# Performance work log

Measured on AMD Instinct MI355X. Metric: run time of the kernel, lower is better.

Reference implementation:

```python
import jax, jax.numpy as jnp
import numpy as np
import math

N = 100000
D = 128       # input_dim
DK = 32       # d_k
H = 4         # heads
DV = D // H   # d_v = 32
DFF = 512     # 4 * input_dim
EPS = 1e-5


def layer_norm(x, g, b):
    mu = jnp.mean(x, axis=-1, keepdims=True)
    var = jnp.var(x, axis=-1, keepdims=True)
    return (x - mu) * jax.lax.rsqrt(var + EPS) * g + b


def setup_inputs() -> dict:
    key = jax.random.key(0)
    ks = jax.random.split(key, 10)
    x = jax.random.normal(ks[0], (N, D), dtype=jnp.float32)
    neighbor_index = jax.random.randint(ks[1], (N, 4), 0, N)
    # xavier-ish scaled params
    w_q = jax.random.normal(ks[2], (H, D, DK), dtype=jnp.float32) * math.sqrt(2.0 / (D + DK))
    w_k = jax.random.normal(ks[3], (H, 5, D, DK), dtype=jnp.float32) * math.sqrt(2.0 / (D + DK))
    w_v = jax.random.normal(ks[4], (H, 5, D, DV), dtype=jnp.float32) * math.sqrt(2.0 / (D + DV))
    W1 = jax.random.normal(ks[5], (D, DFF), dtype=jnp.float32) * math.sqrt(1.0 / D)
    b1 = jnp.zeros((DFF,), dtype=jnp.float32)
    W2 = jax.random.normal(ks[6], (DFF, D), dtype=jnp.float32) * math.sqrt(1.0 / DFF)
    b2 = jnp.zeros((D,), dtype=jnp.float32)
    g1 = jnp.ones((D,), dtype=jnp.float32)
    beta1 = jnp.zeros((D,), dtype=jnp.float32)
    g2 = jnp.ones((D,), dtype=jnp.float32)
    beta2 = jnp.zeros((D,), dtype=jnp.float32)
    return {"x": x, "neighbor_index": neighbor_index, "w_q": w_q, "w_k": w_k,
            "w_v": w_v, "W1": W1, "b1": b1, "W2": W2, "b2": b2,
            "g1": g1, "beta1": beta1, "g2": g2, "beta2": beta2}


def attention(x, neighbor_index, w_q, w_k, w_v):
    # gather the 4 typed neighbors and prepend the self node -> (N, 5, D)
    x_nb = jnp.concatenate([x[:, None, :], x[neighbor_index]], axis=1)
    Q = jnp.einsum('nd,hdk->hnk', x, w_q)                 # (H, N, DK)
    K = jnp.einsum('nrd,hrdk->hnrk', x_nb, w_k)           # (H, N, 5, DK)
    V = jnp.einsum('nrd,hrdv->hnrv', x_nb, w_v)           # (H, N, 5, DV)
    A = jnp.einsum('hnk,hnrk->hnr', Q, K) / math.sqrt(DK)
    # NOTE: original torch code applies softmax over dim=1 (the node axis),
    # reproduced faithfully here.
    A = jax.nn.softmax(A, axis=1)
    Z = jnp.einsum('hnr,hnrv->hnv', A, V)                 # (H, N, DV)
    return jnp.transpose(Z, (1, 0, 2)).reshape(x.shape[0], -1)  # (N, H*DV)


def reference(x, neighbor_index, w_q, w_k, w_v, W1, b1, W2, b2, g1, beta1, g2, beta2):
    attn = attention(x, neighbor_index, w_q, w_k, w_v)
    h = layer_norm(x + attn, g1, beta1)
    ffn = jax.nn.relu(h @ W1 + b1) @ W2 + b2
    return layer_norm(h + ffn, g2, beta2)
```

## Files before the change

### kernel.cpp

```cpp
#include <hip/hip_runtime.h>
#include <hip/hip_bf16.h>

typedef unsigned short u16;
typedef __attribute__((ext_vector_type(8))) short short8;
typedef __attribute__((ext_vector_type(4))) float f32x4;
typedef __attribute__((ext_vector_type(4))) float float4v;
typedef __attribute__((ext_vector_type(4))) unsigned short us4;

#define NN       100000
#define OFF_WK   16384
#define OFF_WV   98304
#define OFF_W1   180224
#define OFF_W2   245760
#define PACK_ELEMS 311296

#define WS_LWS   0u
#define WS_PM    8000000u
#define WS_PS    8000640u
#define WS_MHR   8001280u
#define WS_ISHR  8001408u
#define WS_PK    8001536u
#define WS_XB    8624128u
#define WS_SV    34224128u

static __device__ __forceinline__ float b2f(u16 u){
  unsigned int i = ((unsigned int)u) << 16;
  float f; __builtin_memcpy(&f, &i, 4); return f;
}
static __device__ __forceinline__ u16 f2b(float f){
  unsigned int i; __builtin_memcpy(&i, &f, 4);
  i += 0x7FFFu + ((i >> 16) & 1u);
  return (u16)(i >> 16);
}
static __device__ __forceinline__ f32x4 mfma16(short8 a, short8 b, f32x4 c){
  return __builtin_amdgcn_mfma_f32_16x16x32_bf16(a, b, c, 0, 0, 0);
}
static __device__ __forceinline__ bool detect32(const void* g1){
  return ((const u16*)g1)[0] == 0;
}
static __device__ __forceinline__ float ldf(const void* p, size_t i, bool is32){
  return is32 ? ((const float*)p)[i] : b2f(((const u16*)p)[i]);
}

__global__ __launch_bounds__(256) void k_convert_x(
    const void* __restrict__ x, const void* __restrict__ g1, u16* __restrict__ xb)
{
  const bool is32 = detect32(g1);
  size_t i = (size_t)blockIdx.x * 256 + threadIdx.x;
  us4 o;
  if (is32){
    float4v v = ((const float4v*)x)[i];
    o.x = f2b(v.x); o.y = f2b(v.y); o.z = f2b(v.z); o.w = f2b(v.w);
  } else {
    o = ((const us4*)x)[i];
  }
  ((us4*)xb)[i] = o;
}

__global__ __launch_bounds__(256) void k_convert_small(
    const void* b1, const void* b2, const void* g1, const void* be1,
    const void* g2, const void* be2, u16* __restrict__ sv)
{
  const bool is32 = detect32(g1);
  for (int i = threadIdx.x; i < 1152; i += 256){
    const void* src; int off;
    if      (i < 512) { src = b1;  off = i; }
    else if (i < 640) { src = b2;  off = i - 512; }
    else if (i < 768) { src = g1;  off = i - 640; }
    else if (i < 896) { src = be1; off = i - 768; }
    else if (i < 1024){ src = g2;  off = i - 896; }
    else              { src = be2; off = i - 1024; }
    sv[i] = f2b(ldf(src, off, is32));
  }
}

__global__ __launch_bounds__(256) void k_pack(
    const void* __restrict__ wq, const void* __restrict__ wk,
    const void* __restrict__ wv, const void* __restrict__ W1,
    const void* __restrict__ W2, const void* __restrict__ g1,
    u16* __restrict__ pk)
{
  const bool is32 = detect32(g1);
  int p = blockIdx.x * 256 + threadIdx.x;
  if (p >= PACK_ELEMS) return;
  float v;
  if (p < OFF_WK){
    int q = p;
    int j = q & 7, lane = (q >> 3) & 63, tk = q >> 9;
    int kb = tk & 3, t = tk >> 2;
    int kd = kb*32 + (lane>>4)*8 + j, nc = t*16 + (lane & 15);
    v = ldf(wq, (size_t)(nc>>5)*4096 + kd*32 + (nc & 31), is32);
  } else if (p < OFF_WV){
    int q = p - OFF_WK; int r = q >> 14; q &= 16383;
    int j = q & 7, lane = (q >> 3) & 63, tk = q >> 9;
    int kb = tk & 3, t = tk >> 2;
    int kd = kb*32 + (lane>>4)*8 + j, nc = t*16 + (lane & 15);
    v = ldf(wk, (size_t)((nc>>5)*5 + r)*4096 + kd*32 + (nc & 31), is32);
  } else if (p < OFF_W1){
    int q = p - OFF_WV; int r = q >> 14; q &= 16383;
    int j = q & 7, lane = (q >> 3) & 63, tk = q >> 9;
    int kb = tk & 3, t = tk >> 2;
    int kd = kb*32 + (lane>>4)*8 + j, nc = t*16 + (lane & 15);
    v = ldf(wv, (size_t)((nc>>5)*5 + r)*4096 + kd*32 + (nc & 31), is32);
  } else if (p < OFF_W2){
    int q = p - OFF_W1;
    int j = q & 7, lane = (q >> 3) & 63, tk = q >> 9;
    int kb = tk & 3, t = tk >> 2;
    int kd = kb*32 + (lane>>4)*8 + j, nc = t*16 + (lane & 15);
    v = ldf(W1, (size_t)kd*512 + nc, is32);
  } else {
    int q = p - OFF_W2;
    int j = q & 7, lane = (q >> 3) & 63, tk = q >> 9;
    int c = tk >> 5, t = (tk >> 2) & 7, kb2 = tk & 3;
    int kd = (c*4+kb2)*32 + (lane>>4)*8 + j, nc = t*16 + (lane & 15);
    v = ldf(W2, (size_t)kd*128 + nc, is32);
  }
  pk[p] = f2b(v);
}

__global__ __launch_bounds__(256) void k_qk(
    const u16* __restrict__ x, const int* __restrict__ nbr,
    const u16* __restrict__ pw, float* __restrict__ lws)
{
  __shared__ __align__(16) u16 sbuf[16384];
  const int tid = threadIdx.x, lane = tid & 63, wv = tid >> 6;
  const int m = lane & 15, quad = lane >> 4;
  const int n0 = blockIdx.x * 64 + wv * 16;
  const bool act = (n0 < NN);

  for (int s = tid; s < 2048; s += 256)
    ((short8*)sbuf)[s] = ((const short8*)pw)[s];
  __syncthreads();

  short8 a_self[4];
  f32x4 q[8];
  #pragma unroll
  for (int t = 0; t < 8; t++) q[t] = (f32x4){0.f,0.f,0.f,0.f};
  if (act){
    const short8* xp = (const short8*)(x + (size_t)(n0 + m) * 128);
    #pragma unroll
    for (int kb = 0; kb < 4; kb++) a_self[kb] = xp[kb*4 + quad];
    #pragma unroll
    for (int t = 0; t < 8; t++)
      #pragma unroll
      for (int kb = 0; kb < 4; kb++)
        q[t] = mfma16(a_self[kb], ((const short8*)sbuf)[(t*4+kb)*64 + lane], q[t]);
  }

  for (int r = 0; r < 5; r++){
    __syncthreads();
    for (int s = tid; s < 2048; s += 256)
      ((short8*)sbuf)[s] = ((const short8*)(pw + OFF_WK + (size_t)r*16384))[s];
    __syncthreads();
    if (act){
      short8 a[4];
      if (r == 0){
        #pragma unroll
        for (int kb = 0; kb < 4; kb++) a[kb] = a_self[kb];
      } else {
        int node = nbr[(size_t)(n0 + m)*4 + (r-1)];
        const short8* xp = (const short8*)(x + (size_t)node * 128);
        #pragma unroll
        for (int kb = 0; kb < 4; kb++) a[kb] = xp[kb*4 + quad];
      }
      #pragma unroll
      for (int h = 0; h < 4; h++){
        f32x4 k0 = {0.f,0.f,0.f,0.f}, k1 = {0.f,0.f,0.f,0.f};
        #pragma unroll
        for (int kb = 0; kb < 4; kb++){
          k0 = mfma16(a[kb], ((const short8*)sbuf)[((2*h  )*4+kb)*64 + lane], k0);
          k1 = mfma16(a[kb], ((const short8*)sbuf)[((2*h+1)*4+kb)*64 + lane], k1);
        }
        float p[4];
        #pragma unroll
        for (int i = 0; i < 4; i++) p[i] = q[2*h][i]*k0[i] + q[2*h+1][i]*k1[i];
        #pragma unroll
        for (int mask = 1; mask < 16; mask <<= 1){
          #pragma unroll
          for (int i = 0; i < 4; i++) p[i] += __shfl_xor(p[i], mask, 16);
        }
        if (m == 0){
          #pragma unroll
          for (int i = 0; i < 4; i++)
            lws[(size_t)(h*5+r)*NN + n0 + quad*4 + i] = p[i] * 0.17677669529663687f;
        }
      }
    }
  }
}

__global__ __launch_bounds__(256) void k_red_part(
    const float* __restrict__ lws, float* __restrict__ pm, float* __restrict__ ps)
{
  const int hr = blockIdx.x >> 3, pb = blockIdx.x & 7;
  const int start = pb * 12500, end = start + 12500;
  const float* v = lws + (size_t)hr * NN;
  __shared__ float red[256];
  float mx = -1e30f;
  for (int i = start + threadIdx.x; i < end; i += 256) mx = fmaxf(mx, v[i]);
  red[threadIdx.x] = mx; __syncthreads();
  for (int s = 128; s > 0; s >>= 1){
    if ((int)threadIdx.x < s) red[threadIdx.x] = fmaxf(red[threadIdx.x], red[threadIdx.x+s]);
    __syncthreads();
  }
  mx = red[0]; __syncthreads();
  float sm = 0.f;
  for (int i = start + threadIdx.x; i < end; i += 256) sm += __expf(v[i] - mx);
  red[threadIdx.x] = sm; __syncthreads();
  for (int s = 128; s > 0; s >>= 1){
    if ((int)threadIdx.x < s) red[threadIdx.x] += red[threadIdx.x+s];
    __syncthreads();
  }
  if (threadIdx.x == 0){ pm[blockIdx.x] = mx; ps[blockIdx.x] = red[0]; }
}

__global__ __launch_bounds__(64) void k_red_fin(
    const float* __restrict__ pm, const float* __restrict__ ps,
    float* __restrict__ mhr, float* __restrict__ ishr)
{
  int t = threadIdx.x;
  if (t < 20){
    float M = -1e30f;
    for (int b = 0; b < 8; b++) M = fmaxf(M, pm[t*8+b]);
    float S = 0.f;
    for (int b = 0; b < 8; b++) S += ps[t*8+b] * __expf(pm[t*8+b] - M);
    mhr[t] = M; ishr[t] = 1.0f / S;
  }
}

__global__ __launch_bounds__(256, 2) void k_attn_ffn(
    const u16* __restrict__ x, const void* __restrict__ xraw,
    const int* __restrict__ nbr,
    const u16* __restrict__ pw, const float* __restrict__ lws,
    const float* __restrict__ mhr, const float* __restrict__ ishr,
    const u16* __restrict__ sv, const void* __restrict__ g1raw,
    float* __restrict__ out)
{
  __shared__ __align__(16) u16 sbuf[16384];
  __shared__ __align__(16) u16 hgbuf[16384];
  __shared__ float attw[2560];
  const int tid = threadIdx.x, lane = tid & 63, wv = tid >> 6;
  const int m = lane & 15, quad = lane >> 4;
  const int nblk = blockIdx.x * 128;
  const int n0 = nblk + wv * 32;
  const bool act0 = (n0 < NN), act1 = (n0 + 16 < NN);
  const bool is32 = detect32(g1raw);
  const u16* b1s = sv;
  const u16* b2s = sv + 512;
  const u16* g1s = sv + 640;
  const u16* be1s = sv + 768;
  const u16* g2s = sv + 896;
  const u16* be2s = sv + 1024;

  for (int idx = tid; idx < 2560; idx += 256){
    int tile = idx / 320, rem = idx - tile*320;
    int r = rem >> 6, h = (rem >> 4) & 3, mm = rem & 15, hr = h*5 + r;
    int node = nblk + tile*16 + mm;
    attw[idx] = (node < NN)
        ? __expf(lws[(size_t)hr*NN + node] - mhr[hr]) * ishr[hr] : 0.f;
  }

  f32x4 zacc[2][8];
  #pragma unroll
  for (int tl = 0; tl < 2; tl++)
    #pragma unroll
    for (int t = 0; t < 8; t++) zacc[tl][t] = (f32x4){0.f,0.f,0.f,0.f};

  for (int r = 0; r < 5; r++){
    __syncthreads();
    for (int s = tid; s < 2048; s += 256)
      ((short8*)sbuf)[s] = ((const short8*)(pw + OFF_WV + (size_t)r*16384))[s];
    __syncthreads();

    short8 a2[2][4];
    #pragma unroll
    for (int tl = 0; tl < 2; tl++){
      bool act = tl ? act1 : act0;
      if (!act) continue;
      int rowb = n0 + tl*16;
      if (r == 0){
        const short8* xp = (const short8*)(x + (size_t)(rowb + m) * 128);
        #pragma unroll
        for (int kb = 0; kb < 4; kb++) a2[tl][kb] = xp[kb*4 + quad];
      } else {
        int node = nbr[(size_t)(rowb + m)*4 + (r-1)];
        const short8* xp = (const short8*)(x + (size_t)node * 128);
        #pragma unroll
        for (int kb = 0; kb < 4; kb++) a2[tl][kb] = xp[kb*4 + quad];
      }
    }
    #pragma unroll
    for (int t = 0; t < 8; t++){
      short8 bfr[4];
      #pragma unroll
      for (int kb = 0; kb < 4; kb++)
        bfr[kb] = ((const short8*)sbuf)[(t*4+kb)*64 + lane];
      int h = t >> 1;
      #pragma unroll
      for (int tl = 0; tl < 2; tl++){
        bool act = tl ? act1 : act0;
        if (!act) continue;
        f32x4 v = {0.f,0.f,0.f,0.f};
        #pragma unroll
        for (int kb = 0; kb < 4; kb++) v = mfma16(a2[tl][kb], bfr[kb], v);
        const float* aw = attw + (wv*2+tl)*320 + (r*4+h)*16;
        #pragma unroll
        for (int i = 0; i < 4; i++) zacc[tl][t][i] += aw[quad*4+i] * v[i];
      }
    }
  }
  __syncthreads();

  unsigned int hDp[2][8][2];
  #pragma unroll
  for (int tl = 0; tl < 2; tl++){
    bool act = tl ? act1 : act0;
    if (!act) continue;
    int rowb = n0 + tl*16;
    #pragma unroll
    for (int t = 0; t < 8; t++)
      #pragma unroll
      for (int i = 0; i < 4; i++)
        zacc[tl][t][i] += ldf(xraw, (size_t)(rowb + quad*4 + i)*128 + t*16 + m, is32);
    float s1[4] = {0,0,0,0}, s2[4] = {0,0,0,0};
    #pragma unroll
    for (int t = 0; t < 8; t++)
      #pragma unroll
      for (int i = 0; i < 4; i++){ float y = zacc[tl][t][i]; s1[i] += y; s2[i] += y*y; }
    #pragma unroll
    for (int mask = 1; mask < 16; mask <<= 1){
      #pragma unroll
      for (int i = 0; i < 4; i++){
        s1[i] += __shfl_xor(s1[i], mask, 16);
        s2[i] += __shfl_xor(s2[i], mask, 16);
      }
    }
    float mu[4], rs[4];
    #pragma unroll
    for (int i = 0; i < 4; i++){
      mu[i] = s1[i] * (1.f/128.f);
      float var = s2[i] * (1.f/128.f) - mu[i]*mu[i];
      rs[i] = rsqrtf(var + 1e-5f);
    }
    #pragma unroll
    for (int t = 0; t < 8; t++){
      float gg = b2f(g1s[t*16+m]), bb = b2f(be1s[t*16+m]);
      u16 hv[4];
      #pragma unroll
      for (int i = 0; i < 4; i++){
        hv[i] = f2b((zacc[tl][t][i]-mu[i])*rs[i]*gg + bb);
        hgbuf[(size_t)(wv*32 + tl*16 + quad*4 + i)*128 + t*16 + m] = hv[i];
      }
      hDp[tl][t][0] = (unsigned int)hv[0] | ((unsigned int)hv[1] << 16);
      hDp[tl][t][1] = (unsigned int)hv[2] | ((unsigned int)hv[3] << 16);
    }
  }
  __syncthreads();

  short8 ah[2][4];
  #pragma unroll
  for (int tl = 0; tl < 2; tl++){
    bool act = tl ? act1 : act0;
    if (!act) continue;
    #pragma unroll
    for (int kb = 0; kb < 4; kb++)
      ah[tl][kb] = ((const short8*)hgbuf)[(wv*32 + tl*16 + m)*16 + kb*4 + quad];
  }

  f32x4 f2acc[2][8];
  #pragma unroll
  for (int tl = 0; tl < 2; tl++)
    #pragma unroll
    for (int t = 0; t < 8; t++) f2acc[tl][t] = (f32x4){0.f,0.f,0.f,0.f};

  for (int c = 0; c < 4; c++){
    __syncthreads();
    for (int s = tid; s < 2048; s += 256)
      ((short8*)sbuf)[s] = ((const short8*)(pw + OFF_W1 + (size_t)c*16384))[s];
    __syncthreads();
    #pragma unroll
    for (int t2 = 0; t2 < 8; t2++){
      short8 bfr[4];
      #pragma unroll
      for (int kb = 0; kb < 4; kb++)
        bfr[kb] = ((const short8*)sbuf)[(t2*4+kb)*64 + lane];
      float b1c = b2f(b1s[(c*8+t2)*16 + m]);
      #pragma unroll
      for (int tl = 0; tl < 2; tl++){
        bool act = tl ? act1 : act0;
        if (!act) continue;
        f32x4 g = {0.f,0.f,0.f,0.f};
        #pragma unroll
        for (int kb = 0; kb < 4; kb++) g = mfma16(ah[tl][kb], bfr[kb], g);
        #pragma unroll
        for (int i = 0; i < 4; i++)
          hgbuf[(size_t)(wv*32 + tl*16 + quad*4 + i)*128 + t2*16 + m]
              = f2b(fmaxf(g[i] + b1c, 0.f));
      }
    }
    __syncthreads();
    for (int s = tid; s < 2048; s += 256)
      ((short8*)sbuf)[s] = ((const short8*)(pw + OFF_W2 + (size_t)c*16384))[s];
    short8 ag[2][4];
    #pragma unroll
    for (int tl = 0; tl < 2; tl++){
      bool act = tl ? act1 : act0;
      if (!act) continue;
      #pragma unroll
      for (int kb2 = 0; kb2 < 4; kb2++)
        ag[tl][kb2] = ((const short8*)hgbuf)[(wv*32 + tl*16 + m)*16 + kb2*4 + quad];
    }
    __syncthreads();
    #pragma unroll
    for (int t = 0; t < 8; t++){
      short8 bfr[4];
      #pragma unroll
      for (int kb2 = 0; kb2 < 4; kb2++)
        bfr[kb2] = ((const short8*)sbuf)[(t*4+kb2)*64 + lane];
      #pragma unroll
      for (int tl = 0; tl < 2; tl++){
        bool act = tl ? act1 : act0;
        if (!act) continue;
        #pragma unroll
        for (int kb2 = 0; kb2 < 4; kb2++)
          f2acc[tl][t] = mfma16(ag[tl][kb2], bfr[kb2], f2acc[tl][t]);
      }
    }
  }

  #pragma unroll
  for (int tl = 0; tl < 2; tl++){
    bool act = tl ? act1 : act0;
    if (!act) continue;
    int rowb = n0 + tl*16;
    #pragma unroll
    for (int t = 0; t < 8; t++){
      float b2c = b2f(b2s[t*16 + m]);
      f2acc[tl][t][0] += b2f((u16)(hDp[tl][t][0] & 0xffff)) + b2c;
      f2acc[tl][t][1] += b2f((u16)(hDp[tl][t][0] >> 16))    + b2c;
      f2acc[tl][t][2] += b2f((u16)(hDp[tl][t][1] & 0xffff)) + b2c;
      f2acc[tl][t][3] += b2f((u16)(hDp[tl][t][1] >> 16))    + b2c;
    }
    float s1[4] = {0,0,0,0}, s2[4] = {0,0,0,0};
    #pragma unroll
    for (int t = 0; t < 8; t++)
      #pragma unroll
      for (int i = 0; i < 4; i++){ float y = f2acc[tl][t][i]; s1[i] += y; s2[i] += y*y; }
    #pragma unroll
    for (int mask = 1; mask < 16; mask <<= 1){
      #pragma unroll
      for (int i = 0; i < 4; i++){
        s1[i] += __shfl_xor(s1[i], mask, 16);
        s2[i] += __shfl_xor(s2[i], mask, 16);
      }
    }
    float mu2[4], rs2[4];
    #pragma unroll
    for (int i = 0; i < 4; i++){
      mu2[i] = s1[i] * (1.f/128.f);
      float var = s2[i] * (1.f/128.f) - mu2[i]*mu2[i];
      rs2[i] = rsqrtf(var + 1e-5f);
    }
    #pragma unroll
    for (int t = 0; t < 8; t++){
      float gg = b2f(g2s[t*16+m]), bb = b2f(be2s[t*16+m]);
      #pragma unroll
      for (int i = 0; i < 4; i++)
        out[(size_t)(rowb + quad*4 + i)*128 + t*16 + m] =
            (f2acc[tl][t][i]-mu2[i])*rs2[i]*gg + bb;
    }
  }
}

extern "C" void kernel_launch(void* const* d_in, const int* in_sizes, int n_in,
                              void* d_out, int out_size, void* d_ws, size_t ws_size,
                              hipStream_t stream)
{
  const void* x   = d_in[0];
  const int*  nbr = (const int*)d_in[1];
  const void* wq  = d_in[2];
  const void* wk  = d_in[3];
  const void* wv  = d_in[4];
  const void* W1  = d_in[5];
  const void* b1  = d_in[6];
  const void* W2  = d_in[7];
  const void* b2  = d_in[8];
  const void* g1  = d_in[9];
  const void* be1 = d_in[10];
  const void* g2  = d_in[11];
  const void* be2 = d_in[12];
  float* out = (float*)d_out;

  char* ws = (char*)d_ws;
  float* lws  = (float*)(ws + WS_LWS);
  float* pm   = (float*)(ws + WS_PM);
  float* ps   = (float*)(ws + WS_PS);
  float* mhr  = (float*)(ws + WS_MHR);
  float* ishr = (float*)(ws + WS_ISHR);
  u16*   pk   = (u16*)  (ws + WS_PK);
  u16*   xb   = (u16*)  (ws + WS_XB);
  u16*   sv   = (u16*)  (ws + WS_SV);

  k_convert_x<<<dim3(12500), dim3(256), 0, stream>>>(x, g1, xb);
  k_convert_small<<<dim3(1), dim3(256), 0, stream>>>(b1, b2, g1, be1, g2, be2, sv);
  k_pack<<<dim3((PACK_ELEMS+255)/256), dim3(256), 0, stream>>>(wq, wk, wv, W1, W2, g1, pk);
  k_qk<<<dim3((NN+63)/64), dim3(256), 0, stream>>>(xb, nbr, pk, lws);
  k_red_part<<<dim3(160), dim3(256), 0, stream>>>(lws, pm, ps);
  k_red_fin<<<dim3(1), dim3(64), 0, stream>>>(pm, ps, mhr, ishr);
  k_attn_ffn<<<dim3((NN+127)/128), dim3(256), 0, stream>>>(xb, x, nbr, pk, lws, mhr, ishr,
                                                           sv, g1, out);
}
```

Measured before the change: 314.0 us.

## Fuse FFN chunks through per-wave LDS slices and double rows per wave in QK

The QK kernel now processes 32 rows per wave (two 16-row tiles), so each weight fragment read from shared memory is reused across both tiles, and the grid is halved. The attention+FFN kernel drops its large shared hidden buffer and instead streams W1/W2 fragments interleaved per 32-column slice. Each wave writes its ReLU output into a small padded private LDS slice and immediately feeds it to the W2 MFMAs. The weight packing is reordered to match. This cuts shared memory per block to allow three blocks per CU and removes block-wide syncs around the hidden buffer, at the cost of more weight reload rounds and higher register pressure under the tighter launch bounds.

```diff
diff --git a/kernel.cpp b/kernel.cpp
--- a/kernel.cpp
+++ b/kernel.cpp
@@ -6,12 +6,12 @@
 typedef __attribute__((ext_vector_type(4))) float f32x4;
 typedef __attribute__((ext_vector_type(4))) float float4v;
 typedef __attribute__((ext_vector_type(4))) unsigned short us4;
+typedef __attribute__((ext_vector_type(2))) unsigned int uint2v;
 
 #define NN       100000
 #define OFF_WK   16384
 #define OFF_WV   98304
 #define OFF_W1   180224
-#define OFF_W2   245760
 #define PACK_ELEMS 311296
 
 #define WS_LWS   0u
@@ -23,6 +23,9 @@
 #define WS_XB    8624128u
 #define WS_SV    34224128u
 
+#define PWS_PITCH 36
+#define PWS_SLICE 1280
+
 static __device__ __forceinline__ float b2f(u16 u){
   unsigned int i = ((unsigned int)u) << 16;
   float f; __builtin_memcpy(&f, &i, 4); return f;
@@ -40,6 +43,14 @@
 }
 static __device__ __forceinline__ float ldf(const void* p, size_t i, bool is32){
   return is32 ? ((const float*)p)[i] : b2f(((const u16*)p)[i]);
+}
+static __device__ __forceinline__ short8 lds_afrag(const u16* p){
+  uint2v a = *(const uint2v*)p;
+  uint2v b = *(const uint2v*)(p + 4);
+  short8 r;
+  unsigned int* rp = (unsigned int*)&r;
+  rp[0] = a.x; rp[1] = a.y; rp[2] = b.x; rp[3] = b.y;
+  return r;
 }
 
 __global__ __launch_bounds__(256) void k_convert_x(
@@ -102,49 +113,67 @@
     int kb = tk & 3, t = tk >> 2;
     int kd = kb*32 + (lane>>4)*8 + j, nc = t*16 + (lane & 15);
     v = ldf(wv, (size_t)((nc>>5)*5 + r)*4096 + kd*32 + (nc & 31), is32);
-  } else if (p < OFF_W2){
+  } else {
     int q = p - OFF_W1;
-    int j = q & 7, lane = (q >> 3) & 63, tk = q >> 9;
-    int kb = tk & 3, t = tk >> 2;
-    int kd = kb*32 + (lane>>4)*8 + j, nc = t*16 + (lane & 15);
-    v = ldf(W1, (size_t)kd*512 + nc, is32);
-  } else {
-    int q = p - OFF_W2;
-    int j = q & 7, lane = (q >> 3) & 63, tk = q >> 9;
-    int c = tk >> 5, t = (tk >> 2) & 7, kb2 = tk & 3;
-    int kd = (c*4+kb2)*32 + (lane>>4)*8 + j, nc = t*16 + (lane & 15);
-    v = ldf(W2, (size_t)kd*128 + nc, is32);
+    int j = q & 7, lane = (q >> 3) & 63, rest = q >> 9;
+    int pairIdx = rest >> 4, sub = rest & 15;
+    int c = pairIdx >> 2, kb2 = pairIdx & 3;
+    int half = lane >> 4, mc = lane & 15;
+    if (sub < 8){
+      int u = sub >> 2, kb = sub & 3;
+      int kd = kb*32 + half*8 + j;
+      int nc = c*128 + (kb2*2+u)*16 + mc;
+      v = ldf(W1, (size_t)kd*512 + nc, is32);
+    } else {
+      int t = sub - 8;
+      int kd = (c*4+kb2)*32 + half*8 + j;
+      int nc = t*16 + mc;
+      v = ldf(W2, (size_t)kd*128 + nc, is32);
+    }
   }
   pk[p] = f2b(v);
 }
 
-__global__ __launch_bounds__(256) void k_qk(
+__global__ __launch_bounds__(256, 3) void k_qk(
     const u16* __restrict__ x, const int* __restrict__ nbr,
     const u16* __restrict__ pw, float* __restrict__ lws)
 {
   __shared__ __align__(16) u16 sbuf[16384];
   const int tid = threadIdx.x, lane = tid & 63, wv = tid >> 6;
   const int m = lane & 15, quad = lane >> 4;
-  const int n0 = blockIdx.x * 64 + wv * 16;
-  const bool act = (n0 < NN);
-
+  const int n0 = blockIdx.x * 128 + wv * 32;
+  const bool act0 = (n0 < NN), act1 = (n0 + 16 < NN);
+
+  const short8* sb8 = (const short8*)sbuf;
   for (int s = tid; s < 2048; s += 256)
     ((short8*)sbuf)[s] = ((const short8*)pw)[s];
   __syncthreads();
 
-  short8 a_self[4];
-  f32x4 q[8];
-  #pragma unroll
-  for (int t = 0; t < 8; t++) q[t] = (f32x4){0.f,0.f,0.f,0.f};
-  if (act){
-    const short8* xp = (const short8*)(x + (size_t)(n0 + m) * 128);
-    #pragma unroll
-    for (int kb = 0; kb < 4; kb++) a_self[kb] = xp[kb*4 + quad];
-    #pragma unroll
-    for (int t = 0; t < 8; t++)
-      #pragma unroll
-      for (int kb = 0; kb < 4; kb++)
-        q[t] = mfma16(a_self[kb], ((const short8*)sbuf)[(t*4+kb)*64 + lane], q[t]);
+  short8 a[2][4];
+  f32x4 q[2][8];
+  #pragma unroll
+  for (int tl = 0; tl < 2; tl++)
+    #pragma unroll
+    for (int t = 0; t < 8; t++) q[tl][t] = (f32x4){0.f,0.f,0.f,0.f};
+
+  #pragma unroll
+  for (int tl = 0; tl < 2; tl++){
+    if (!(tl ? act1 : act0)) continue;
+    const short8* xp = (const short8*)(x + (size_t)(n0 + tl*16 + m) * 128);
+    #pragma unroll
+    for (int kb = 0; kb < 4; kb++) a[tl][kb] = xp[kb*4 + quad];
+  }
+  #pragma unroll
+  for (int t = 0; t < 8; t++){
+    short8 bfr[4];
+    #pragma unroll
+    for (int kb = 0; kb < 4; kb++) bfr[kb] = sb8[(t*4+kb)*64 + lane];
+    #pragma unroll
+    for (int tl = 0; tl < 2; tl++){
+      if (!(tl ? act1 : act0)) continue;
+      #pragma unroll
+      for (int kb = 0; kb < 4; kb++) q[tl][t] = mfma16(a[tl][kb], bfr[kb], q[tl][t]);
+    }
   }
 
   for (int r = 0; r < 5; r++){
@@ -152,28 +181,36 @@
     for (int s = tid; s < 2048; s += 256)
       ((short8*)sbuf)[s] = ((const short8*)(pw + OFF_WK + (size_t)r*16384))[s];
     __syncthreads();
-    if (act){
-      short8 a[4];
-      if (r == 0){
-        #pragma unroll
-        for (int kb = 0; kb < 4; kb++) a[kb] = a_self[kb];
-      } else {
-        int node = nbr[(size_t)(n0 + m)*4 + (r-1)];
+    if (r > 0){
+      #pragma unroll
+      for (int tl = 0; tl < 2; tl++){
+        if (!(tl ? act1 : act0)) continue;
+        int node = nbr[(size_t)(n0 + tl*16 + m)*4 + (r-1)];
         const short8* xp = (const short8*)(x + (size_t)node * 128);
         #pragma unroll
-        for (int kb = 0; kb < 4; kb++) a[kb] = xp[kb*4 + quad];
-      }
-      #pragma unroll
-      for (int h = 0; h < 4; h++){
+        for (int kb = 0; kb < 4; kb++) a[tl][kb] = xp[kb*4 + quad];
+      }
+    }
+    #pragma unroll
+    for (int h = 0; h < 4; h++){
+      short8 b0[4], b1f[4];
+      #pragma unroll
+      for (int kb = 0; kb < 4; kb++){
+        b0[kb]  = sb8[((2*h  )*4+kb)*64 + lane];
+        b1f[kb] = sb8[((2*h+1)*4+kb)*64 + lane];
+      }
+      #pragma unroll
+      for (int tl = 0; tl < 2; tl++){
+        if (!(tl ? act1 : act0)) continue;
         f32x4 k0 = {0.f,0.f,0.f,0.f}, k1 = {0.f,0.f,0.f,0.f};
         #pragma unroll
         for (int kb = 0; kb < 4; kb++){
-          k0 = mfma16(a[kb], ((const short8*)sbuf)[((2*h  )*4+kb)*64 + lane], k0);
-          k1 = mfma16(a[kb], ((const short8*)sbuf)[((2*h+1)*4+kb)*64 + lane], k1);
+          k0 = mfma16(a[tl][kb], b0[kb],  k0);
+          k1 = mfma16(a[tl][kb], b1f[kb], k1);
         }
         float p[4];
         #pragma unroll
-        for (int i = 0; i < 4; i++) p[i] = q[2*h][i]*k0[i] + q[2*h+1][i]*k1[i];
+        for (int i = 0; i < 4; i++) p[i] = q[tl][2*h][i]*k0[i] + q[tl][2*h+1][i]*k1[i];
         #pragma unroll
         for (int mask = 1; mask < 16; mask <<= 1){
           #pragma unroll
@@ -182,7 +219,8 @@
         if (m == 0){
           #pragma unroll
           for (int i = 0; i < 4; i++)
-            lws[(size_t)(h*5+r)*NN + n0 + quad*4 + i] = p[i] * 0.17677669529663687f;
+            lws[(size_t)(h*5+r)*NN + n0 + tl*16 + quad*4 + i]
+                = p[i] * 0.17677669529663687f;
         }
       }
     }
@@ -228,7 +266,7 @@
   }
 }
 
-__global__ __launch_bounds__(256, 2) void k_attn_ffn(
+__global__ __launch_bounds__(256, 3) void k_attn_ffn(
     const u16* __restrict__ x, const void* __restrict__ xraw,
     const int* __restrict__ nbr,
     const u16* __restrict__ pw, const float* __restrict__ lws,
@@ -237,12 +275,10 @@
     float* __restrict__ out)
 {
   __shared__ __align__(16) u16 sbuf[16384];
-  __shared__ __align__(16) u16 hgbuf[16384];
-  __shared__ float attw[2560];
+  __shared__ __align__(16) u16 upool[5120];
   const int tid = threadIdx.x, lane = tid & 63, wv = tid >> 6;
   const int m = lane & 15, quad = lane >> 4;
-  const int nblk = blockIdx.x * 128;
-  const int n0 = nblk + wv * 32;
+  const int n0 = blockIdx.x * 128 + wv * 32;
   const bool act0 = (n0 < NN), act1 = (n0 + 16 < NN);
   const bool is32 = detect32(g1raw);
   const u16* b1s = sv;
@@ -251,12 +287,15 @@
   const u16* be1s = sv + 768;
   const u16* g2s = sv + 896;
   const u16* be2s = sv + 1024;
-
-  for (int idx = tid; idx < 2560; idx += 256){
-    int tile = idx / 320, rem = idx - tile*320;
+  const short8* sb8 = (const short8*)sbuf;
+  float* attw_w = ((float*)upool) + wv * 640;
+  u16*   pws_w  = upool + wv * PWS_SLICE;
+
+  for (int j = lane; j < 640; j += 64){
+    int tl = j / 320, rem = j - tl*320;
     int r = rem >> 6, h = (rem >> 4) & 3, mm = rem & 15, hr = h*5 + r;
-    int node = nblk + tile*16 + mm;
-    attw[idx] = (node < NN)
+    int node = n0 + tl*16 + mm;
+    attw_w[j] = (node < NN)
         ? __expf(lws[(size_t)hr*NN + node] - mhr[hr]) * ishr[hr] : 0.f;
   }
 
@@ -266,56 +305,49 @@
     #pragma unroll
     for (int t = 0; t < 8; t++) zacc[tl][t] = (f32x4){0.f,0.f,0.f,0.f};
 
+  short8 a2[2][4];
   for (int r = 0; r < 5; r++){
     __syncthreads();
     for (int s = tid; s < 2048; s += 256)
       ((short8*)sbuf)[s] = ((const short8*)(pw + OFF_WV + (size_t)r*16384))[s];
     __syncthreads();
 
-    short8 a2[2][4];
     #pragma unroll
     for (int tl = 0; tl < 2; tl++){
-      bool act = tl ? act1 : act0;
-      if (!act) continue;
+      if (!(tl ? act1 : act0)) continue;
       int rowb = n0 + tl*16;
-      if (r == 0){
-        const short8* xp = (const short8*)(x + (size_t)(rowb + m) * 128);
-        #pragma unroll
-        for (int kb = 0; kb < 4; kb++) a2[tl][kb] = xp[kb*4 + quad];
-      } else {
+      const short8* xp;
+      if (r == 0) xp = (const short8*)(x + (size_t)(rowb + m) * 128);
+      else {
         int node = nbr[(size_t)(rowb + m)*4 + (r-1)];
-        const short8* xp = (const short8*)(x + (size_t)node * 128);
-        #pragma unroll
-        for (int kb = 0; kb < 4; kb++) a2[tl][kb] = xp[kb*4 + quad];
-      }
+        xp = (const short8*)(x + (size_t)node * 128);
+      }
+      #pragma unroll
+      for (int kb = 0; kb < 4; kb++) a2[tl][kb] = xp[kb*4 + quad];
     }
     #pragma unroll
     for (int t = 0; t < 8; t++){
       short8 bfr[4];
       #pragma unroll
-      for (int kb = 0; kb < 4; kb++)
-        bfr[kb] = ((const short8*)sbuf)[(t*4+kb)*64 + lane];
+      for (int kb = 0; kb < 4; kb++) bfr[kb] = sb8[(t*4+kb)*64 + lane];
       int h = t >> 1;
       #pragma unroll
       for (int tl = 0; tl < 2; tl++){
-        bool act = tl ? act1 : act0;
-        if (!act) continue;
+        if (!(tl ? act1 : act0)) continue;
         f32x4 v = {0.f,0.f,0.f,0.f};
         #pragma unroll
         for (int kb = 0; kb < 4; kb++) v = mfma16(a2[tl][kb], bfr[kb], v);
-        const float* aw = attw + (wv*2+tl)*320 + (r*4+h)*16;
+        const float* aw = attw_w + tl*320 + (r*4+h)*16;
         #pragma unroll
         for (int i = 0; i < 4; i++) zacc[tl][t][i] += aw[quad*4+i] * v[i];
       }
     }
   }
-  __syncthreads();
-
-  unsigned int hDp[2][8][2];
+
+  float mu[2][4], rs[2][4];
   #pragma unroll
   for (int tl = 0; tl < 2; tl++){
-    bool act = tl ? act1 : act0;
-    if (!act) continue;
+    if (!(tl ? act1 : act0)) continue;
     int rowb = n0 + tl*16;
     #pragma unroll
     for (int t = 0; t < 8; t++)
@@ -335,103 +367,96 @@
         s2[i] += __shfl_xor(s2[i], mask, 16);
       }
     }
-    float mu[4], rs[4];
     #pragma unroll
     for (int i = 0; i < 4; i++){
-      mu[i] = s1[i] * (1.f/128.f);
-      float var = s2[i] * (1.f/128.f) - mu[i]*mu[i];
-      rs[i] = rsqrtf(var + 1e-5f);
-    }
-    #pragma unroll
-    for (int t = 0; t < 8; t++){
-      float gg = b2f(g1s[t*16+m]), bb = b2f(be1s[t*16+m]);
-      u16 hv[4];
-      #pragma unroll
-      for (int i = 0; i < 4; i++){
-        hv[i] = f2b((zacc[tl][t][i]-mu[i])*rs[i]*gg + bb);
-        hgbuf[(size_t)(wv*32 + tl*16 + quad*4 + i)*128 + t*16 + m] = hv[i];
-      }
-      hDp[tl][t][0] = (unsigned int)hv[0] | ((unsigned int)hv[1] << 16);
-      hDp[tl][t][1] = (unsigned int)hv[2] | ((unsigned int)hv[3] << 16);
-    }
-  }
-  __syncthreads();
-
+      mu[tl][i] = s1[i] * (1.f/128.f);
+      float var = s2[i] * (1.f/128.f) - mu[tl][i]*mu[tl][i];
+      rs[tl][i] = rsqrtf(var + 1e-5f);
+    }
+  }
+
+  unsigned int hDp[2][8][2];
   short8 ah[2][4];
   #pragma unroll
+  for (int kb = 0; kb < 4; kb++){
+    #pragma unroll
+    for (int u = 0; u < 2; u++){
+      int t = kb*2 + u;
+      #pragma unroll
+      for (int tl = 0; tl < 2; tl++){
+        if (!(tl ? act1 : act0)) continue;
+        float gg = b2f(g1s[t*16+m]), bb = b2f(be1s[t*16+m]);
+        u16 hv[4];
+        #pragma unroll
+        for (int i = 0; i < 4; i++){
+          hv[i] = f2b((zacc[tl][t][i]-mu[tl][i])*rs[tl][i]*gg + bb);
+          pws_w[(tl*16 + quad*4 + i)*PWS_PITCH + u*16 + m] = hv[i];
+        }
+        hDp[tl][t][0] = (unsigned int)hv[0] | ((unsigned int)hv[1] << 16);
+        hDp[tl][t][1] = (unsigned int)hv[2] | ((unsigned int)hv[3] << 16);
+      }
+    }
+    #pragma unroll
+    for (int tl = 0; tl < 2; tl++)
+      ah[tl][kb] = lds_afrag(pws_w + (tl*16 + m)*PWS_PITCH + quad*8);
+  }
+
+  f32x4 f2acc[2][8];
+  #pragma unroll
+  for (int tl = 0; tl < 2; tl++)
+    #pragma unroll
+    for (int t = 0; t < 8; t++) f2acc[tl][t] = (f32x4){0.f,0.f,0.f,0.f};
+
+  for (int c = 0; c < 4; c++){
+    for (int kp = 0; kp < 2; kp++){
+      __syncthreads();
+      for (int s = tid; s < 2048; s += 256)
+        ((short8*)sbuf)[s] =
+            ((const short8*)(pw + OFF_W1 + (size_t)(c*4 + kp*2)*8192))[s];
+      __syncthreads();
+      #pragma unroll
+      for (int kb2w = 0; kb2w < 2; kb2w++){
+        int kb2 = kp*2 + kb2w;
+        const short8* w1f = sb8 + kb2w*1024;
+        const short8* w2f = w1f + 512;
+        #pragma unroll
+        for (int u = 0; u < 2; u++){
+          short8 bfr[4];
+          #pragma unroll
+          for (int kb = 0; kb < 4; kb++) bfr[kb] = w1f[(u*4+kb)*64 + lane];
+          float b1c = b2f(b1s[c*128 + (kb2*2+u)*16 + m]);
+          #pragma unroll
+          for (int tl = 0; tl < 2; tl++){
+            if (!(tl ? act1 : act0)) continue;
+            f32x4 g = {0.f,0.f,0.f,0.f};
+            #pragma unroll
+            for (int kb = 0; kb < 4; kb++) g = mfma16(ah[tl][kb], bfr[kb], g);
+            #pragma unroll
+            for (int i = 0; i < 4; i++)
+              pws_w[(tl*16 + quad*4 + i)*PWS_PITCH + u*16 + m]
+                  = f2b(fmaxf(g[i] + b1c, 0.f));
+          }
+        }
+        short8 ag[2];
+        #pragma unroll
+        for (int tl = 0; tl < 2; tl++)
+          ag[tl] = lds_afrag(pws_w + (tl*16 + m)*PWS_PITCH + quad*8);
+        #pragma unroll
+        for (int t = 0; t < 8; t++){
+          short8 bf = w2f[t*64 + lane];
+          #pragma unroll
+          for (int tl = 0; tl < 2; tl++){
+            if (!(tl ? act1 : act0)) continue;
+            f2acc[tl][t] = mfma16(ag[tl], bf, f2acc[tl][t]);
+          }
+        }
+      }
+    }
+  }
+
+  #pragma unroll
   for (int tl = 0; tl < 2; tl++){
-    bool act = tl ? act1 : act0;
-    if (!act) continue;
-    #pragma unroll
-    for (int kb = 0; kb < 4; kb++)
-      ah[tl][kb] = ((const short8*)hgbuf)[(wv*32 + tl*16 + m)*16 + kb*4 + quad];
-  }
-
-  f32x4 f2acc[2][8];
-  #pragma unroll
-  for (int tl = 0; tl < 2; tl++)
-    #pragma unroll
-    for (int t = 0; t < 8; t++) f2acc[tl][t] = (f32x4){0.f,0.f,0.f,0.f};
-
-  for (int c = 0; c < 4; c++){
-    __syncthreads();
-    for (int s = tid; s < 2048; s += 256)
-      ((short8*)sbuf)[s] = ((const short8*)(pw + OFF_W1 + (size_t)c*16384))[s];
-    __syncthreads();
-    #pragma unroll
-    for (int t2 = 0; t2 < 8; t2++){
-      short8 bfr[4];
-      #pragma unroll
-      for (int kb = 0; kb < 4; kb++)
-        bfr[kb] = ((const short8*)sbuf)[(t2*4+kb)*64 + lane];
-      float b1c = b2f(b1s[(c*8+t2)*16 + m]);
-      #pragma unroll
-      for (int tl = 0; tl < 2; tl++){
-        bool act = tl ? act1 : act0;
-        if (!act) continue;
-        f32x4 g = {0.f,0.f,0.f,0.f};
-        #pragma unroll
-        for (int kb = 0; kb < 4; kb++) g = mfma16(ah[tl][kb], bfr[kb], g);
-        #pragma unroll
-        for (int i = 0; i < 4; i++)
-          hgbuf[(size_t)(wv*32 + tl*16 + quad*4 + i)*128 + t2*16 + m]
-              = f2b(fmaxf(g[i] + b1c, 0.f));
-      }
-    }
-    __syncthreads();
-    for (int s = tid; s < 2048; s += 256)
-      ((short8*)sbuf)[s] = ((const short8*)(pw + OFF_W2 + (size_t)c*16384))[s];
-    short8 ag[2][4];
-    #pragma unroll
-    for (int tl = 0; tl < 2; tl++){
-      bool act = tl ? act1 : act0;
-      if (!act) continue;
-      #pragma unroll
-      for (int kb2 = 0; kb2 < 4; kb2++)
-        ag[tl][kb2] = ((const short8*)hgbuf)[(wv*32 + tl*16 + m)*16 + kb2*4 + quad];
-    }
-    __syncthreads();
-    #pragma unroll
-    for (int t = 0; t < 8; t++){
-      short8 bfr[4];
-      #pragma unroll
-      for (int kb2 = 0; kb2 < 4; kb2++)
-        bfr[kb2] = ((const short8*)sbuf)[(t*4+kb2)*64 + lane];
-      #pragma unroll
-      for (int tl = 0; tl < 2; tl++){
-        bool act = tl ? act1 : act0;
-        if (!act) continue;
-        #pragma unroll
-        for (int kb2 = 0; kb2 < 4; kb2++)
-          f2acc[tl][t] = mfma16(ag[tl][kb2], bfr[kb2], f2acc[tl][t]);
-      }
-    }
-  }
-
-  #pragma unroll
-  for (int tl = 0; tl < 2; tl++){
-    bool act = tl ? act1 : act0;
-    if (!act) continue;
+    if (!(tl ? act1 : act0)) continue;
     int rowb = n0 + tl*16;
     #pragma unroll
     for (int t = 0; t < 8; t++){
@@ -504,7 +529,7 @@
   k_convert_x<<<dim3(12500), dim3(256), 0, stream>>>(x, g1, xb);
   k_convert_small<<<dim3(1), dim3(256), 0, stream>>>(b1, b2, g1, be1, g2, be2, sv);
   k_pack<<<dim3((PACK_ELEMS+255)/256), dim3(256), 0, stream>>>(wq, wk, wv, W1, W2, g1, pk);
-  k_qk<<<dim3((NN+63)/64), dim3(256), 0, stream>>>(xb, nbr, pk, lws);
+  k_qk<<<dim3((NN+127)/128), dim3(256), 0, stream>>>(xb, nbr, pk, lws);
   k_red_part<<<dim3(160), dim3(256), 0, stream>>>(lws, pm, ps);
   k_red_fin<<<dim3(1), dim3(64), 0, stream>>>(pm, ps, mhr, ishr);
   k_attn_ffn<<<dim3((NN+127)/128), dim3(256), 0, stream>>>(xb, x, nbr, pk, lws, mhr, ishr,
```

New measurement: 353.1 us. 1.12x slower.
